# Optimization experiments

Hardware: AMD Instinct MI355X
Metric: run time of the kernel (lower is better)

## Reference

```python
import jax, jax.numpy as jnp
import numpy as np

SELECTOR = jnp.array([29, 49, 79])
N_FINAL = 6
N_EM_ITERS = 10
LOG_2PI = float(np.log(2.0 * np.pi))


def _logdet2(c):
    # log determinant of trailing 2x2 matrices
    return jnp.log(c[..., 0, 0] * c[..., 1, 1] - c[..., 0, 1] * c[..., 1, 0])


def _inv2(c):
    # analytic inverse of trailing 2x2 matrices
    det = c[..., 0, 0] * c[..., 1, 1] - c[..., 0, 1] * c[..., 1, 0]
    inv = jnp.stack([
        jnp.stack([c[..., 1, 1], -c[..., 0, 1]], axis=-1),
        jnp.stack([-c[..., 1, 0], c[..., 0, 0]], axis=-1),
    ], axis=-2)
    return inv / det[..., None, None]


def _initial_state(probas, trajectories):
    B, M = probas.shape
    tsel = trajectories[:, :, SELECTOR, :]                       # [B,M,3,2]
    dots = jnp.einsum('bmtd,bntd->btmn', tsel, tsel)             # [B,3,M,M]
    d1 = jnp.einsum('bmtd,bmtd->btm', tsel, tsel)                # [B,3,M]
    R = jnp.sqrt(d1[:, :, :, None] + d1[:, :, None, :] - 2.0 * dots)
    thr = jnp.quantile(R[:, -1].reshape(B, -1), 0.15, axis=-1)[:, None, None, None]
    adj = (R <= thr).astype(probas.dtype).prod(axis=1)           # [B,M,M]
    worked = jnp.ones((B, M), dtype=probas.dtype)
    bidx = jnp.arange(B)
    idxs = []
    for _ in range(N_FINAL):
        score = (adj * probas[:, None, :]).sum(axis=2) * worked  # [B,M]
        amax = jnp.argmax(score, axis=-1)                        # [B]
        worked = worked * (1.0 - adj[bidx, amax])
        idxs.append(amax)
    return jnp.stack(idxs, axis=1)                               # [B,6]


def _coefficients(cov6, trajectories, traj6, probas6):
    cov6_sel = cov6[:, :, SELECTOR]                              # [B,6,3,2,2]
    prec = _inv2(cov6_sel)                                       # [B,6,3,2,2]
    diff = traj6[:, :, SELECTOR][:, :, None] - trajectories[:, :, SELECTOR][:, None]  # [B,6,M,3,2]
    qform = jnp.einsum('bnmti,bntij,bnmtj->bnmt', diff, prec, diff)
    logdet = _logdet2(cov6_sel)[:, :, None, :]                   # [B,6,1,3]
    pM = jnp.exp((-LOG_2PI - 0.5 * logdet - 0.5 * qform).sum(axis=-1)) + 1e-8  # [B,6,M]
    num = pM * probas6[:, :, None]
    return num / (num.sum(axis=1, keepdims=True) + 1e-8)


def _forward(non_normalized_probas, trajectories, covariance_matrices):
    B = trajectories.shape[0]
    probas = jax.nn.softmax(non_normalized_probas, axis=-1)
    idx = jax.lax.stop_gradient(_initial_state(probas, trajectories))  # [B,6]
    b = jnp.arange(B)[:, None]
    traj6 = trajectories[b, idx]                                 # [B,6,T,2]
    probas6 = jax.nn.softmax(jnp.take_along_axis(non_normalized_probas, idx, axis=1), axis=-1)
    cov6 = covariance_matrices[b, idx]                           # [B,6,T,2,2]
    for _ in range(N_EM_ITERS):
        pM = jax.lax.stop_gradient(_coefficients(cov6, trajectories, traj6, probas6))
        P = probas[:, None, :] * pM                              # [B,6,M]
        probas6 = P.sum(axis=-1)                                 # [B,6]
        traj6 = jnp.einsum('bnm,bmtd->bntd', P, trajectories) / probas6[:, :, None, None]
        diff = traj6[:, :, None] - trajectories[:, None]         # [B,6,M,T,2]
        cov6 = (jnp.einsum('bnm,bmtij->bntij', P, covariance_matrices)
                + jnp.einsum('bnm,bnmti,bnmtj->bntij', P, diff, diff)) / probas6[:, :, None, None, None]
    return probas6, traj6, cov6


def setup_inputs() -> dict:
    key = jax.random.key(0)
    k1, k2, k3 = jax.random.split(key, 3)
    B, M, T = 256, 48, 80
    logits = jax.random.normal(k1, (B, M), dtype=jnp.float32)
    trajectories = jax.random.normal(k2, (B, M, T, 2), dtype=jnp.float32)
    A = 0.3 * jax.random.normal(k3, (B, M, T, 2, 2), dtype=jnp.float32)
    cov = A @ jnp.swapaxes(A, -1, -2) + 0.5 * jnp.eye(2, dtype=jnp.float32)
    return {'non_normalized_probas': logits, 'trajectories': trajectories,
            'covariance_matrices': cov}


def reference(non_normalized_probas, trajectories, covariance_matrices):
    return _forward(non_normalized_probas, trajectories, covariance_matrices)
```

## Files before the change

### kernel.cpp

```cpp
#include <hip/hip_runtime.h>
#include <math.h>

#define BATCH 256
#define M 48
#define T 80
#define NF 6
#define EMIT 10
#define MM (M*M)
#define KPL (MM/64)
#define LOG2PI 1.8378770664093453f

typedef unsigned int u32;
typedef unsigned long long u64;

__global__ __launch_bounds__(256, 1)
void em_kernel(const float* __restrict__ g_logits,
               const float* __restrict__ g_traj,
               const float* __restrict__ g_cov,
               float* __restrict__ g_out)
{
    const int b = blockIdx.x;
    const int tid = threadIdx.x;
    const int lane = tid & 63;
    const int wv = tid >> 6;
    const int SEL[3] = {29, 49, 79};

    __shared__ __align__(16) float s_txy[M*T*2];
    __shared__ __align__(16) float s_cv4[M*T*4];
    __shared__ float s_adj[MM];
    __shared__ float s_logits[M];
    __shared__ float s_probas[M];
    __shared__ float s_tsel[M*6];
    __shared__ float s_d1[M*3];
    __shared__ __align__(16) float s_csel[M*3*4];
    __shared__ __align__(16) float s_Pm[4][M*8];
    __shared__ float s_t6sel[4][NF*6];
    __shared__ float s_probas6[4][NF];
    __shared__ float s_prec[4][NF*3*3];
    __shared__ float s_ld[4][NF*3];
    __shared__ int   s_idx[4][8];
    __shared__ __align__(16) u32 s_hist[4][256];

    const float* traj_b = g_traj + (size_t)b*(M*T*2);
    const float* cov_b  = g_cov  + (size_t)b*(M*T*4);

    float myLogit = -1e30f;
    if (lane < M) myLogit = g_logits[b*M + lane];
    float selx[3], sely[3], cc0[3], cc1[3], cc2[3];
    #pragma unroll
    for (int r = 0; r < 3; ++r) {
        int i = lane + r*64;
        if (i < M*3) {
            int m = i/3, tt = i - (i/3)*3;
            float2 xy = ((const float2*)traj_b)[m*T + SEL[tt]];
            float4 cv = ((const float4*)cov_b)[m*T + SEL[tt]];
            selx[r]=xy.x; sely[r]=xy.y; cc0[r]=cv.x; cc1[r]=cv.y; cc2[r]=cv.w;
        }
    }

    __builtin_amdgcn_sched_barrier(0);
    {
        const char* gt = (const char*)traj_b + lane*16;
        char* lt = (char*)s_txy;
        #pragma unroll 2
        for (int k = wv; k < 30; k += 4)
            __builtin_amdgcn_global_load_lds(
                (const __attribute__((address_space(1))) u32*)(gt + k*1024),
                (__attribute__((address_space(3))) u32*)(lt + k*1024), 16, 0, 0);
        const char* gc = (const char*)cov_b + lane*16;
        char* lc = (char*)s_cv4;
        #pragma unroll 2
        for (int k = wv; k < 60; k += 4)
            __builtin_amdgcn_global_load_lds(
                (const __attribute__((address_space(1))) u32*)(gc + k*1024),
                (__attribute__((address_space(3))) u32*)(lc + k*1024), 16, 0, 0);
    }
    __builtin_amdgcn_sched_barrier(0);

    if (lane < M) s_logits[lane] = myLogit;
    #pragma unroll
    for (int r = 0; r < 3; ++r) {
        int i = lane + r*64;
        if (i < M*3) {
            int m = i/3, tt = i - (i/3)*3;
            s_tsel[m*6+tt*2+0] = selx[r];
            s_tsel[m*6+tt*2+1] = sely[r];
            s_d1[i] = selx[r]*selx[r] + sely[r]*sely[r];
            s_csel[i*4+0]=cc0[r]; s_csel[i*4+1]=cc1[r]; s_csel[i*4+2]=cc2[r]; s_csel[i*4+3]=0.f;
        }
    }

    float mx = myLogit;
    #pragma unroll
    for (int off = 32; off; off >>= 1) mx = fmaxf(mx, __shfl_xor(mx, off));
    float pe = (lane < M) ? __expf(myLogit - mx) : 0.f;
    float psum = pe;
    #pragma unroll
    for (int off = 32; off; off >>= 1) psum += __shfl_xor(psum, off);
    const float proba = pe / psum;
    if (lane < M) s_probas[lane] = proba;

    u32 key[KPL];
    #pragma unroll
    for (int c = 0; c < KPL; ++c) {
        int e = lane + c*64;
        int m = e/M, n = e - (e/M)*M;
        float dot = s_tsel[m*6+4]*s_tsel[n*6+4] + s_tsel[m*6+5]*s_tsel[n*6+5];
        float v = s_d1[m*3+2] + s_d1[n*3+2] - 2.0f*dot;
        key[c] = __float_as_uint(sqrtf(fmaxf(v, 0.0f)));
    }

    u32* hist = &s_hist[wv][0];
    int target = 345;
    u32 prefix = 0u, pmask = 0u;
    #pragma unroll 1
    for (int shift = 24; shift >= 0; shift -= 8) {
        ((uint4*)hist)[lane] = make_uint4(0,0,0,0);
        #pragma unroll
        for (int c = 0; c < KPL; ++c) {
            if ((key[c] & pmask) == prefix)
                atomicAdd(&hist[(key[c] >> shift) & 255u], 1u);
        }
        uint4 hv = ((const uint4*)hist)[lane];
        u32 s4 = hv.x + hv.y + hv.z + hv.w;
        u32 cum = s4;
        #pragma unroll
        for (int off = 1; off < 64; off <<= 1) {
            u32 u = __shfl_up(cum, off);
            if (lane >= off) cum += u;
        }
        u64 bmask = __ballot(cum > (u32)target);
        int g = __builtin_ctzll(bmask);
        int dig = 0; u32 binstart = 0;
        if (lane == g) {
            u32 exc = cum - s4;
            int bi2 = lane*4;
            if (exc + hv.x > (u32)target)      { dig = bi2;   binstart = exc; }
            else { exc += hv.x;
                if (exc + hv.y > (u32)target)  { dig = bi2+1; binstart = exc; }
                else { exc += hv.y;
                    if (exc + hv.z > (u32)target) { dig = bi2+2; binstart = exc; }
                    else { exc += hv.z;            dig = bi2+3; binstart = exc; } } }
        }
        dig = __shfl(dig, g);
        binstart = (u32)__shfl((int)binstart, g);
        target -= (int)binstart;
        prefix |= ((u32)dig) << shift;
        pmask  |= (255u << shift);
    }
    const u32 k1 = prefix;
    const float v1f = __uint_as_float(k1);

    float v2f;
    {
        u32 cnt = 0, mng = 0xFFFFFFFFu;
        #pragma unroll
        for (int c = 0; c < KPL; ++c) {
            if (key[c] <= k1) cnt++;
            else mng = (key[c] < mng) ? key[c] : mng;
        }
        #pragma unroll
        for (int off = 32; off > 0; off >>= 1) {
            cnt += __shfl_down(cnt, off);
            u32 mo = (u32)__shfl_down((int)mng, off);
            mng = (mo < mng) ? mo : mng;
        }
        u32 ct = (u32)__shfl((int)cnt, 0);
        u32 mt = (u32)__shfl((int)mng, 0);
        v2f = (ct >= 347u) ? v1f : __uint_as_float(mt);
    }
    const float qi = 0.15f * 2303.0f;
    const float fr = qi - floorf(qi);
    const float thr = v1f*(1.0f - fr) + v2f*fr;

    #pragma unroll
    for (int c = 0; c < KPL; ++c) {
        int e = lane + c*64;
        int m = e/M, n = e - (e/M)*M;
        float d0 = s_tsel[m*6+0]*s_tsel[n*6+0] + s_tsel[m*6+1]*s_tsel[n*6+1];
        float r0 = sqrtf(fmaxf(s_d1[m*3+0] + s_d1[n*3+0] - 2.0f*d0, 0.0f));
        float d1v = s_tsel[m*6+2]*s_tsel[n*6+2] + s_tsel[m*6+3]*s_tsel[n*6+3];
        float r1 = sqrtf(fmaxf(s_d1[m*3+1] + s_d1[n*3+1] - 2.0f*d1v, 0.0f));
        bool a = (__uint_as_float(key[c]) <= thr) && (r0 <= thr) && (r1 <= thr);
        s_adj[e] = a ? 1.0f : 0.0f;
    }

    const int m = (lane < M) ? lane : (M-1);
    {
        float base = 0.f;
        #pragma unroll
        for (int n = 0; n < M; ++n) base += s_adj[n*M+m] * s_probas[n];
        float worked = 1.f;
        #pragma unroll 1
        for (int k = 0; k < NF; ++k) {
            float sc = (lane < M) ? base*worked : -1.f;
            int bi = lane;
            #pragma unroll
            for (int off = 32; off; off >>= 1) {
                float so = __shfl_down(sc, off);
                int io = __shfl_down(bi, off);
                if (so > sc || (so == sc && io < bi)) { sc = so; bi = io; }
            }
            int amax = __shfl(bi, 0);
            if (lane == 0) s_idx[wv][k] = amax;
            worked *= (1.f - s_adj[amax*M+m]);
        }
    }

    if (lane < NF) {
        float mx6 = -1e30f;
        #pragma unroll
        for (int j = 0; j < NF; ++j) mx6 = fmaxf(mx6, s_logits[s_idx[wv][j]]);
        float sum6 = 0.f;
        #pragma unroll
        for (int j = 0; j < NF; ++j) sum6 += __expf(s_logits[s_idx[wv][j]] - mx6);
        s_probas6[wv][lane] = __expf(s_logits[s_idx[wv][lane]] - mx6) / sum6;
    }
    if (lane < NF*3) {
        int n = lane/3, tt = lane - (lane/3)*3;
        int m0 = s_idx[wv][n];
        s_t6sel[wv][n*6+tt*2+0] = s_tsel[m0*6+tt*2+0];
        s_t6sel[wv][n*6+tt*2+1] = s_tsel[m0*6+tt*2+1];
        float c00 = s_csel[(m0*3+tt)*4+0];
        float c01 = s_csel[(m0*3+tt)*4+1];
        float c11 = s_csel[(m0*3+tt)*4+2];
        float det = c00*c11 - c01*c01;
        s_prec[wv][lane*3+0] =  c11/det;
        s_prec[wv][lane*3+1] = -c01/det;
        s_prec[wv][lane*3+2] =  c00/det;
        s_ld[wv][lane] = __logf(det);
    }

    float tm0=s_tsel[m*6+0], tm1=s_tsel[m*6+1], tm2=s_tsel[m*6+2],
          tm3=s_tsel[m*6+3], tm4=s_tsel[m*6+4], tm5=s_tsel[m*6+5];
    const int item  = lane/3;
    const int chunk = lane - item*3;
    const int mn    = item/3;
    const int mtt   = item - (item/3)*3;
    const int mslot = (mn < 3) ? mn : mn + 1;

    #pragma unroll 1
    for (int it = 0; it < EMIT; ++it) {
        float num[NF]; float den = 1e-8f;
        #pragma unroll
        for (int n = 0; n < NF; ++n) {
            float lsum = s_ld[wv][n*3+0] + s_ld[wv][n*3+1] + s_ld[wv][n*3+2];
            float dx0 = s_t6sel[wv][n*6+0]-tm0, dy0 = s_t6sel[wv][n*6+1]-tm1;
            float dx1 = s_t6sel[wv][n*6+2]-tm2, dy1 = s_t6sel[wv][n*6+3]-tm3;
            float dx2 = s_t6sel[wv][n*6+4]-tm4, dy2 = s_t6sel[wv][n*6+5]-tm5;
            float q = s_prec[wv][(n*3+0)*3+0]*dx0*dx0 + 2.f*s_prec[wv][(n*3+0)*3+1]*dx0*dy0 + s_prec[wv][(n*3+0)*3+2]*dy0*dy0
                    + s_prec[wv][(n*3+1)*3+0]*dx1*dx1 + 2.f*s_prec[wv][(n*3+1)*3+1]*dx1*dy1 + s_prec[wv][(n*3+1)*3+2]*dy1*dy1
                    + s_prec[wv][(n*3+2)*3+0]*dx2*dx2 + 2.f*s_prec[wv][(n*3+2)*3+1]*dx2*dy2 + s_prec[wv][(n*3+2)*3+2]*dy2*dy2;
            num[n] = (__expf(-3.f*LOG2PI - 0.5f*lsum - 0.5f*q) + 1e-8f) * s_probas6[wv][n];
            den += num[n];
        }
        float f = proba / den;
        if (lane < M) {
            *(float4*)&s_Pm[wv][m*8]   = make_float4(num[0]*f, num[1]*f, num[2]*f, 0.f);
            *(float4*)&s_Pm[wv][m*8+4] = make_float4(num[3]*f, num[4]*f, num[5]*f, 0.f);
        }
        if (it == EMIT-1) break;

        if (lane < 54) {
            float SP=0,S1x=0,S1y=0,Sxx=0,Sxy=0,Syy=0,Cs0=0,Cs1=0,Cs2=0;
            int mbase = chunk*16;
            #pragma unroll 4
            for (int k = 0; k < 16; ++k) {
                int mm = mbase + k;
                float p = s_Pm[wv][mm*8 + mslot];
                float x = s_tsel[mm*6+mtt*2+0];
                float y = s_tsel[mm*6+mtt*2+1];
                float4 c4 = *(const float4*)&s_csel[(mm*3+mtt)*4];
                SP += p; S1x += p*x; S1y += p*y;
                Sxx += p*x*x; Sxy += p*x*y; Syy += p*y*y;
                Cs0 += p*c4.x; Cs1 += p*c4.y; Cs2 += p*c4.z;
            }
            #define CMB(v) { float a1_=__shfl_down(v,1), a2_=__shfl_down(v,2); v += a1_ + a2_; }
            CMB(SP) CMB(S1x) CMB(S1y) CMB(Sxx) CMB(Sxy) CMB(Syy) CMB(Cs0) CMB(Cs1) CMB(Cs2)
            if (chunk == 0) {
                float p6 = SP;
                if (mtt == 0) s_probas6[wv][mn] = SP;
                float tx = S1x/p6, ty = S1y/p6;
                float c00 = (Cs0 + (Sxx - S1x*tx)) / p6;
                float c01 = (Cs1 + (Sxy - S1x*ty)) / p6;
                float c11 = (Cs2 + (Syy - S1y*ty)) / p6;
                float det = c00*c11 - c01*c01;
                s_prec[wv][item*3+0] =  c11/det;
                s_prec[wv][item*3+1] = -c01/det;
                s_prec[wv][item*3+2] =  c00/det;
                s_ld[wv][item] = __logf(det);
                s_t6sel[wv][mn*6+mtt*2+0] = tx;
                s_t6sel[wv][mn*6+mtt*2+1] = ty;
            }
        }
    }

    __syncthreads();

    float*  out_p = g_out;
    float2* out_t = (float2*)(g_out + BATCH*NF);
    float4* out_c = (float4*)(g_out + BATCH*NF + BATCH*NF*T*2);
    if (lane < 40) {
        int it2 = wv*40 + lane;
        int t = it2 >> 1, half = it2 & 1;
        float SP[3]={0,0,0}, S1x[3]={0,0,0}, S1y[3]={0,0,0};
        float Sxx[3]={0,0,0}, Sxy[3]={0,0,0}, Syy[3]={0,0,0};
        float C00[3]={0,0,0}, C01[3]={0,0,0}, C11[3]={0,0,0};
        #pragma unroll 4
        for (int mm = 0; mm < M; ++mm) {
            float2 xy = ((const float2*)s_txy)[mm*T + t];
            float4 c4 = ((const float4*)s_cv4)[mm*T + t];
            float4 pq = *(const float4*)&s_Pm[wv][mm*8 + half*4];
            float p[3] = {pq.x, pq.y, pq.z};
            float xx = xy.x*xy.x, xyv = xy.x*xy.y, yy = xy.y*xy.y;
            #pragma unroll
            for (int j = 0; j < 3; ++j) {
                SP[j]+=p[j]; S1x[j]+=p[j]*xy.x; S1y[j]+=p[j]*xy.y;
                Sxx[j]+=p[j]*xx; Sxy[j]+=p[j]*xyv; Syy[j]+=p[j]*yy;
                C00[j]+=p[j]*c4.x; C01[j]+=p[j]*c4.y; C11[j]+=p[j]*c4.w;
            }
        }
        #pragma unroll
        for (int j = 0; j < 3; ++j) {
            int n = half*3 + j;
            float p6 = SP[j];
            float tx = S1x[j]/p6, ty = S1y[j]/p6;
            float c00 = (C00[j] + (Sxx[j] - S1x[j]*tx)) / p6;
            float c01 = (C01[j] + (Sxy[j] - S1x[j]*ty)) / p6;
            float c11 = (C11[j] + (Syy[j] - S1y[j]*ty)) / p6;
            size_t o = (size_t)(b*NF + n)*T + t;
            out_t[o] = make_float2(tx, ty);
            out_c[o] = make_float4(c00, c01, c01, c11);
        }
    }
    if (wv == 0 && lane < NF) {
        int slot = (lane < 3) ? lane : lane + 1;
        float sp = 0.f;
        for (int mm = 0; mm < M; ++mm) sp += s_Pm[0][mm*8 + slot];
        out_p[b*NF + lane] = sp;
    }
}

extern "C" void kernel_launch(void* const* d_in, const int* in_sizes, int n_in,
                              void* d_out, int out_size, void* d_ws, size_t ws_size,
                              hipStream_t stream) {
    const float* logits = (const float*)d_in[0];
    const float* traj   = (const float*)d_in[1];
    const float* cov    = (const float*)d_in[2];
    float* out = (float*)d_out;
    em_kernel<<<dim3(BATCH), dim3(256), 0, stream>>>(logits, traj, cov, out);
}
```

Measured before the change: 122.3 us.

## Share EM M-step across the workgroup with double-buffered params and drop sqrt from quantile keys

Before this change, each of the four waves ran its own copy of the EM iterations with private per-wave shared state. Now the M-step is split across the whole workgroup: 18 groups of 8 threads each reduce 6 mixtures, with parameters double-buffered and a raw s_barrier after each iteration. The quantile radix-select now runs on squared distances, taking sqrt only on the selected values and converting the threshold back to an exact squared-domain bound. Several divides become fast reciprocals. The trade is shorter per-iteration reduction chains and fewer sqrts in exchange for workgroup barriers inside the EM loop and lower-precision divides.

```diff
diff --git a/kernel.cpp b/kernel.cpp
--- a/kernel.cpp
+++ b/kernel.cpp
@@ -12,6 +12,9 @@
 
 typedef unsigned int u32;
 typedef unsigned long long u64;
+
+#define WGSYNC()     __asm__ __volatile__("s_waitcnt lgkmcnt(0)\ns_barrier" ::: "memory")
+#define WGSYNC_ALL() __asm__ __volatile__("s_waitcnt vmcnt(0) lgkmcnt(0)\ns_barrier" ::: "memory")
 
 __global__ __launch_bounds__(256, 1)
 void em_kernel(const float* __restrict__ g_logits,
@@ -33,12 +36,12 @@
     __shared__ float s_tsel[M*6];
     __shared__ float s_d1[M*3];
     __shared__ __align__(16) float s_csel[M*3*4];
-    __shared__ __align__(16) float s_Pm[4][M*8];
-    __shared__ float s_t6sel[4][NF*6];
-    __shared__ float s_probas6[4][NF];
-    __shared__ float s_prec[4][NF*3*3];
-    __shared__ float s_ld[4][NF*3];
-    __shared__ int   s_idx[4][8];
+    __shared__ __align__(16) float s_Pm[M*8];
+    __shared__ float s_t6sel[2][NF*6];
+    __shared__ float s_probas6[2][NF];
+    __shared__ float s_prec[2][NF*3*3];
+    __shared__ float s_ld[2][NF*3];
+    __shared__ int   s_idx[8];
     __shared__ __align__(16) u32 s_hist[4][256];
 
     const float* traj_b = g_traj + (size_t)b*(M*T*2);
@@ -107,7 +110,7 @@
         int m = e/M, n = e - (e/M)*M;
         float dot = s_tsel[m*6+4]*s_tsel[n*6+4] + s_tsel[m*6+5]*s_tsel[n*6+5];
         float v = s_d1[m*3+2] + s_d1[n*3+2] - 2.0f*dot;
-        key[c] = __float_as_uint(sqrtf(fmaxf(v, 0.0f)));
+        key[c] = __float_as_uint(fmaxf(v, 0.0f));
     }
 
     u32* hist = &s_hist[wv][0];
@@ -149,7 +152,7 @@
         pmask  |= (255u << shift);
     }
     const u32 k1 = prefix;
-    const float v1f = __uint_as_float(k1);
+    const float v1f = sqrtf(__uint_as_float(k1));
 
     float v2f;
     {
@@ -167,21 +170,29 @@
         }
         u32 ct = (u32)__shfl((int)cnt, 0);
         u32 mt = (u32)__shfl((int)mng, 0);
-        v2f = (ct >= 347u) ? v1f : __uint_as_float(mt);
+        v2f = (ct >= 347u) ? v1f : sqrtf(__uint_as_float(mt));
     }
     const float qi = 0.15f * 2303.0f;
     const float fr = qi - floorf(qi);
     const float thr = v1f*(1.0f - fr) + v2f*fr;
+
+    float dthr;
+    {
+        u32 ub = __float_as_uint(thr*thr);
+        while (sqrtf(__uint_as_float(ub)) > thr) --ub;
+        while (sqrtf(__uint_as_float(ub+1u)) <= thr) ++ub;
+        dthr = __uint_as_float(ub);
+    }
 
     #pragma unroll
     for (int c = 0; c < KPL; ++c) {
         int e = lane + c*64;
         int m = e/M, n = e - (e/M)*M;
         float d0 = s_tsel[m*6+0]*s_tsel[n*6+0] + s_tsel[m*6+1]*s_tsel[n*6+1];
-        float r0 = sqrtf(fmaxf(s_d1[m*3+0] + s_d1[n*3+0] - 2.0f*d0, 0.0f));
+        float v0 = fmaxf(s_d1[m*3+0] + s_d1[n*3+0] - 2.0f*d0, 0.0f);
         float d1v = s_tsel[m*6+2]*s_tsel[n*6+2] + s_tsel[m*6+3]*s_tsel[n*6+3];
-        float r1 = sqrtf(fmaxf(s_d1[m*3+1] + s_d1[n*3+1] - 2.0f*d1v, 0.0f));
-        bool a = (__uint_as_float(key[c]) <= thr) && (r0 <= thr) && (r1 <= thr);
+        float v1 = fmaxf(s_d1[m*3+1] + s_d1[n*3+1] - 2.0f*d1v, 0.0f);
+        bool a = (__uint_as_float(key[c]) <= dthr) && (v0 <= dthr) && (v1 <= dthr);
         s_adj[e] = a ? 1.0f : 0.0f;
     }
 
@@ -202,7 +213,7 @@
                 if (so > sc || (so == sc && io < bi)) { sc = so; bi = io; }
             }
             int amax = __shfl(bi, 0);
-            if (lane == 0) s_idx[wv][k] = amax;
+            if (lane == 0) s_idx[k] = amax;
             worked *= (1.f - s_adj[amax*M+m]);
         }
     }
@@ -210,92 +221,101 @@
     if (lane < NF) {
         float mx6 = -1e30f;
         #pragma unroll
-        for (int j = 0; j < NF; ++j) mx6 = fmaxf(mx6, s_logits[s_idx[wv][j]]);
+        for (int j = 0; j < NF; ++j) mx6 = fmaxf(mx6, s_logits[s_idx[j]]);
         float sum6 = 0.f;
         #pragma unroll
-        for (int j = 0; j < NF; ++j) sum6 += __expf(s_logits[s_idx[wv][j]] - mx6);
-        s_probas6[wv][lane] = __expf(s_logits[s_idx[wv][lane]] - mx6) / sum6;
+        for (int j = 0; j < NF; ++j) sum6 += __expf(s_logits[s_idx[j]] - mx6);
+        s_probas6[0][lane] = __expf(s_logits[s_idx[lane]] - mx6) / sum6;
     }
     if (lane < NF*3) {
         int n = lane/3, tt = lane - (lane/3)*3;
-        int m0 = s_idx[wv][n];
-        s_t6sel[wv][n*6+tt*2+0] = s_tsel[m0*6+tt*2+0];
-        s_t6sel[wv][n*6+tt*2+1] = s_tsel[m0*6+tt*2+1];
+        int m0 = s_idx[n];
+        s_t6sel[0][n*6+tt*2+0] = s_tsel[m0*6+tt*2+0];
+        s_t6sel[0][n*6+tt*2+1] = s_tsel[m0*6+tt*2+1];
         float c00 = s_csel[(m0*3+tt)*4+0];
         float c01 = s_csel[(m0*3+tt)*4+1];
         float c11 = s_csel[(m0*3+tt)*4+2];
         float det = c00*c11 - c01*c01;
-        s_prec[wv][lane*3+0] =  c11/det;
-        s_prec[wv][lane*3+1] = -c01/det;
-        s_prec[wv][lane*3+2] =  c00/det;
-        s_ld[wv][lane] = __logf(det);
+        float rdet = __fdividef(1.0f, det);
+        s_prec[0][lane*3+0] =  c11*rdet;
+        s_prec[0][lane*3+1] = -c01*rdet;
+        s_prec[0][lane*3+2] =  c00*rdet;
+        s_ld[0][lane] = __logf(det);
     }
 
     float tm0=s_tsel[m*6+0], tm1=s_tsel[m*6+1], tm2=s_tsel[m*6+2],
           tm3=s_tsel[m*6+3], tm4=s_tsel[m*6+4], tm5=s_tsel[m*6+5];
-    const int item  = lane/3;
-    const int chunk = lane - item*3;
-    const int mn    = item/3;
-    const int mtt   = item - (item/3)*3;
-    const int mslot = (mn < 3) ? mn : mn + 1;
+    const int gid = tid >> 3;
+    const int sub = tid & 7;
+    const int gn  = gid/3, gtt = gid - (gid/3)*3;
+    const int gslot = (gn < 3) ? gn : gn + 1;
 
     #pragma unroll 1
     for (int it = 0; it < EMIT; ++it) {
+        const int cur = it & 1, nxt = cur ^ 1;
+        const float* prC = s_prec[cur];
+        const float* ldC = s_ld[cur];
+        const float* t6C = s_t6sel[cur];
+        const float* p6C = s_probas6[cur];
+
         float num[NF]; float den = 1e-8f;
         #pragma unroll
         for (int n = 0; n < NF; ++n) {
-            float lsum = s_ld[wv][n*3+0] + s_ld[wv][n*3+1] + s_ld[wv][n*3+2];
-            float dx0 = s_t6sel[wv][n*6+0]-tm0, dy0 = s_t6sel[wv][n*6+1]-tm1;
-            float dx1 = s_t6sel[wv][n*6+2]-tm2, dy1 = s_t6sel[wv][n*6+3]-tm3;
-            float dx2 = s_t6sel[wv][n*6+4]-tm4, dy2 = s_t6sel[wv][n*6+5]-tm5;
-            float q = s_prec[wv][(n*3+0)*3+0]*dx0*dx0 + 2.f*s_prec[wv][(n*3+0)*3+1]*dx0*dy0 + s_prec[wv][(n*3+0)*3+2]*dy0*dy0
-                    + s_prec[wv][(n*3+1)*3+0]*dx1*dx1 + 2.f*s_prec[wv][(n*3+1)*3+1]*dx1*dy1 + s_prec[wv][(n*3+1)*3+2]*dy1*dy1
-                    + s_prec[wv][(n*3+2)*3+0]*dx2*dx2 + 2.f*s_prec[wv][(n*3+2)*3+1]*dx2*dy2 + s_prec[wv][(n*3+2)*3+2]*dy2*dy2;
-            num[n] = (__expf(-3.f*LOG2PI - 0.5f*lsum - 0.5f*q) + 1e-8f) * s_probas6[wv][n];
+            float lsum = ldC[n*3+0] + ldC[n*3+1] + ldC[n*3+2];
+            float dx0 = t6C[n*6+0]-tm0, dy0 = t6C[n*6+1]-tm1;
+            float dx1 = t6C[n*6+2]-tm2, dy1 = t6C[n*6+3]-tm3;
+            float dx2 = t6C[n*6+4]-tm4, dy2 = t6C[n*6+5]-tm5;
+            float q = prC[(n*3+0)*3+0]*dx0*dx0 + 2.f*prC[(n*3+0)*3+1]*dx0*dy0 + prC[(n*3+0)*3+2]*dy0*dy0
+                    + prC[(n*3+1)*3+0]*dx1*dx1 + 2.f*prC[(n*3+1)*3+1]*dx1*dy1 + prC[(n*3+1)*3+2]*dy1*dy1
+                    + prC[(n*3+2)*3+0]*dx2*dx2 + 2.f*prC[(n*3+2)*3+1]*dx2*dy2 + prC[(n*3+2)*3+2]*dy2*dy2;
+            num[n] = (__expf(-3.f*LOG2PI - 0.5f*lsum - 0.5f*q) + 1e-8f) * p6C[n];
             den += num[n];
         }
-        float f = proba / den;
+        float f = __fdividef(proba, den);
         if (lane < M) {
-            *(float4*)&s_Pm[wv][m*8]   = make_float4(num[0]*f, num[1]*f, num[2]*f, 0.f);
-            *(float4*)&s_Pm[wv][m*8+4] = make_float4(num[3]*f, num[4]*f, num[5]*f, 0.f);
+            *(float4*)&s_Pm[m*8]   = make_float4(num[0]*f, num[1]*f, num[2]*f, 0.f);
+            *(float4*)&s_Pm[m*8+4] = make_float4(num[3]*f, num[4]*f, num[5]*f, 0.f);
         }
         if (it == EMIT-1) break;
 
-        if (lane < 54) {
-            float SP=0,S1x=0,S1y=0,Sxx=0,Sxy=0,Syy=0,Cs0=0,Cs1=0,Cs2=0;
-            int mbase = chunk*16;
-            #pragma unroll 4
-            for (int k = 0; k < 16; ++k) {
-                int mm = mbase + k;
-                float p = s_Pm[wv][mm*8 + mslot];
-                float x = s_tsel[mm*6+mtt*2+0];
-                float y = s_tsel[mm*6+mtt*2+1];
-                float4 c4 = *(const float4*)&s_csel[(mm*3+mtt)*4];
+        if (gid < 18) {
+            float SP=0,S1x=0,S1y=0,Sxx=0,Sxy=0,Syy=0,C0=0,C1=0,C2=0;
+            #pragma unroll
+            for (int k = 0; k < 6; ++k) {
+                int mm = sub*6 + k;
+                float p = s_Pm[mm*8 + gslot];
+                float x = s_tsel[mm*6+gtt*2+0];
+                float y = s_tsel[mm*6+gtt*2+1];
+                float4 c4 = *(const float4*)&s_csel[(mm*3+gtt)*4];
                 SP += p; S1x += p*x; S1y += p*y;
                 Sxx += p*x*x; Sxy += p*x*y; Syy += p*y*y;
-                Cs0 += p*c4.x; Cs1 += p*c4.y; Cs2 += p*c4.z;
+                C0 += p*c4.x; C1 += p*c4.y; C2 += p*c4.z;
             }
-            #define CMB(v) { float a1_=__shfl_down(v,1), a2_=__shfl_down(v,2); v += a1_ + a2_; }
-            CMB(SP) CMB(S1x) CMB(S1y) CMB(Sxx) CMB(Sxy) CMB(Syy) CMB(Cs0) CMB(Cs1) CMB(Cs2)
-            if (chunk == 0) {
+            #define R8(v) { v += __shfl_down(v,4); v += __shfl_down(v,2); v += __shfl_down(v,1); }
+            R8(SP) R8(S1x) R8(S1y) R8(Sxx) R8(Sxy) R8(Syy) R8(C0) R8(C1) R8(C2)
+            #undef R8
+            if (sub == 0) {
                 float p6 = SP;
-                if (mtt == 0) s_probas6[wv][mn] = SP;
-                float tx = S1x/p6, ty = S1y/p6;
-                float c00 = (Cs0 + (Sxx - S1x*tx)) / p6;
-                float c01 = (Cs1 + (Sxy - S1x*ty)) / p6;
-                float c11 = (Cs2 + (Syy - S1y*ty)) / p6;
+                float tx = __fdividef(S1x, p6), ty = __fdividef(S1y, p6);
+                float rp = __fdividef(1.0f, p6);
+                float c00 = (C0 + (Sxx - S1x*tx)) * rp;
+                float c01 = (C1 + (Sxy - S1x*ty)) * rp;
+                float c11 = (C2 + (Syy - S1y*ty)) * rp;
                 float det = c00*c11 - c01*c01;
-                s_prec[wv][item*3+0] =  c11/det;
-                s_prec[wv][item*3+1] = -c01/det;
-                s_prec[wv][item*3+2] =  c00/det;
-                s_ld[wv][item] = __logf(det);
-                s_t6sel[wv][mn*6+mtt*2+0] = tx;
-                s_t6sel[wv][mn*6+mtt*2+1] = ty;
+                float rdet = __fdividef(1.0f, det);
+                s_prec[nxt][gid*3+0] =  c11*rdet;
+                s_prec[nxt][gid*3+1] = -c01*rdet;
+                s_prec[nxt][gid*3+2] =  c00*rdet;
+                s_ld[nxt][gid] = __logf(det);
+                s_t6sel[nxt][gn*6+gtt*2+0] = tx;
+                s_t6sel[nxt][gn*6+gtt*2+1] = ty;
+                if (gtt == 0) s_probas6[nxt][gn] = SP;
             }
         }
-    }
-
-    __syncthreads();
+        WGSYNC();
+    }
+
+    WGSYNC_ALL();
 
     float*  out_p = g_out;
     float2* out_t = (float2*)(g_out + BATCH*NF);
@@ -310,7 +330,7 @@
         for (int mm = 0; mm < M; ++mm) {
             float2 xy = ((const float2*)s_txy)[mm*T + t];
             float4 c4 = ((const float4*)s_cv4)[mm*T + t];
-            float4 pq = *(const float4*)&s_Pm[wv][mm*8 + half*4];
+            float4 pq = *(const float4*)&s_Pm[mm*8 + half*4];
             float p[3] = {pq.x, pq.y, pq.z};
             float xx = xy.x*xy.x, xyv = xy.x*xy.y, yy = xy.y*xy.y;
             #pragma unroll
@@ -324,10 +344,11 @@
         for (int j = 0; j < 3; ++j) {
             int n = half*3 + j;
             float p6 = SP[j];
-            float tx = S1x[j]/p6, ty = S1y[j]/p6;
-            float c00 = (C00[j] + (Sxx[j] - S1x[j]*tx)) / p6;
-            float c01 = (C01[j] + (Sxy[j] - S1x[j]*ty)) / p6;
-            float c11 = (C11[j] + (Syy[j] - S1y[j]*ty)) / p6;
+            float tx = __fdividef(S1x[j], p6), ty = __fdividef(S1y[j], p6);
+            float rp = __fdividef(1.0f, p6);
+            float c00 = (C00[j] + (Sxx[j] - S1x[j]*tx)) * rp;
+            float c01 = (C01[j] + (Sxy[j] - S1x[j]*ty)) * rp;
+            float c11 = (C11[j] + (Syy[j] - S1y[j]*ty)) * rp;
             size_t o = (size_t)(b*NF + n)*T + t;
             out_t[o] = make_float2(tx, ty);
             out_c[o] = make_float4(c00, c01, c01, c11);
@@ -336,7 +357,7 @@
     if (wv == 0 && lane < NF) {
         int slot = (lane < 3) ? lane : lane + 1;
         float sp = 0.f;
-        for (int mm = 0; mm < M; ++mm) sp += s_Pm[0][mm*8 + slot];
+        for (int mm = 0; mm < M; ++mm) sp += s_Pm[mm*8 + slot];
         out_p[b*NF + lane] = sp;
     }
 }
```

After: 113.0 us. -7.7%, faster.
